# Performance work log

Measured on AMD Instinct MI355X. Metric: run time of the kernel, lower is better.

## Reference

```python
import jax, jax.numpy as jnp
import numpy as np

B, C, T = 8, 512, 8192
NQ, CBS, CBD = 9, 1024, 8
EPS = 1e-12  # F.normalize eps


def setup_inputs() -> dict:
    key = jax.random.key(0)
    ks = jax.random.split(key, 12)
    n = lambda i, shape, s: jax.random.normal(ks[i], shape, jnp.float32) * s
    return {
        "z": n(0, (B, C, T), 1.0),
        "down_w": n(1, (2, C, C, 2), 0.02),   # [layer, out, in, k] (torch Conv1d layout)
        "down_b": n(2, (2, C), 0.01),
        "up_w": n(3, (2, C, C, 2), 0.02),     # [layer, in, out, k] (torch ConvTranspose1d layout)
        "up_b": n(4, (2, C), 0.01),
        "in_v": n(5, (NQ, CBD, C), 0.05),     # weight_norm direction of in_proj 1x1 conv
        "in_g": 1.0 + n(6, (NQ, CBD), 0.02),  # weight_norm magnitude
        "in_b": n(7, (NQ, CBD), 0.01),
        "out_v": n(8, (NQ, C, CBD), 0.05),
        "out_g": 1.0 + n(9, (NQ, C), 0.02),
        "out_b": n(10, (NQ, C), 0.01),
        "codebooks": n(11, (NQ, CBS, CBD), 1.0),
    }


def _wn(g, v):
    # weight_norm (dim=0): per-output-row rescale
    return g[:, None] * v / jnp.linalg.norm(v, axis=1, keepdims=True)


def _l2norm(x):
    return x / jnp.maximum(jnp.linalg.norm(x, axis=-1, keepdims=True), EPS)


def _forward(z, down_w, down_b, up_w, up_b, in_v, in_g, in_b, out_v, out_g, out_b, codebooks):
    # --- downsample: two Conv1d(k=2, s=2) ---
    x = z
    for l in range(2):
        b, c, t = x.shape
        xr = x.reshape(b, c, t // 2, 2)
        x = jnp.einsum('bitk,oik->bot', xr, down_w[l]) + down_b[l][None, :, None]

    residual = x
    z_q = jnp.zeros_like(x)
    commit_loss = jnp.float32(0.0)
    cb_loss = jnp.float32(0.0)
    codes = []
    for i in range(NQ):
        # in_proj 1x1 conv (weight-normed)
        w_in = _wn(in_g[i], in_v[i])                 # [CBD, C]
        z_e = jnp.einsum('bdt,cd->bct', residual, w_in) + in_b[i][None, :, None]  # [B, CBD, T']
        # decode_latents: L2-normalize + squared-euclid via matmul + argmax
        bt = z_e.shape[0] * z_e.shape[2]
        enc = z_e.transpose(0, 2, 1).reshape(bt, CBD)
        enc_n = _l2norm(enc)
        cbk = codebooks[i]
        cb_n = _l2norm(cbk)
        dist = ((enc_n ** 2).sum(1, keepdims=True)
                - 2.0 * enc_n @ cb_n.T
                + (cb_n ** 2).sum(1)[None, :])        # [B*T', CBS]
        idx = jnp.argmax(-dist, axis=1).reshape(z_e.shape[0], -1)  # [B, T']
        z_q_i = cbk[idx].transpose(0, 2, 1)           # [B, CBD, T'] (un-normalized codebook rows)
        # losses (eval: mask all-true -> per-batch mean over (1,2) then batch mean == global mean)
        commit_loss = commit_loss + ((z_e - jax.lax.stop_gradient(z_q_i)) ** 2).mean()
        cb_loss = cb_loss + ((z_q_i - jax.lax.stop_gradient(z_e)) ** 2).mean()
        # straight-through + out_proj 1x1 conv (weight-normed)
        z_st = z_e + jax.lax.stop_gradient(z_q_i - z_e)
        w_out = _wn(out_g[i], out_v[i])               # [C, CBD]
        z_q_out = jnp.einsum('bct,dc->bdt', z_st, w_out) + out_b[i][None, :, None]
        z_q = z_q + z_q_out
        residual = residual - z_q_out
        codes.append(idx)
    codes = jnp.stack(codes, axis=1)                  # [B, NQ, T']

    x = z_q
    for l in range(2):
        b, c, t = x.shape
        x = jnp.einsum('bit,iok->botk', x, up_w[l]).reshape(b, C, t * 2) + up_b[l][None, :, None]
    return x, codes, commit_loss, cb_loss


def reference(z, down_w, down_b, up_w, up_b, in_v, in_g, in_b, out_v, out_g, out_b, codebooks):
    return _forward(z, down_w, down_b, up_w, up_b, in_v, in_g, in_b, out_v, out_g, out_b, codebooks)
```

## Files before the change

kernel.cpp:

```cpp
#include <hip/hip_runtime.h>
#include <math.h>


using u16 = unsigned short;
typedef __attribute__((ext_vector_type(8))) short bf16x8;
typedef __attribute__((ext_vector_type(8))) u16 su16x8;
typedef __attribute__((ext_vector_type(4))) float f32x4;

constexpr int NQ = 9, CBS = 1024, CBD = 8;
constexpr int TQ = 2048;
constexpr int NTOK = 16384;
constexpr int APS = 1048576;
#define EPSN 1e-12f

constexpr size_t OFF_X2    = 0;
constexpr size_t OFF_E0T   = 8388608;
constexpr size_t OFF_Q     = 9568256;
constexpr size_t OFF_WD    = 10878976;
constexpr size_t OFF_WDP   = 11927552;
constexpr size_t OFF_WEFF  = 13500416;
constexpr size_t OFF_WX    = 14548992;
constexpr size_t OFF_WINN  = 14712832;
constexpr size_t OFF_WOUTS = 14749696;
constexpr size_t OFF_CBS   = 14790656;
constexpr size_t OFF_PT    = 14809088;
constexpr size_t OFF_BEFF  = 14811428;
constexpr size_t OFF_BSUM  = 14811500;
constexpr size_t OFF_BD    = 14812012;
constexpr size_t OFF_BUP   = 14812524;
constexpr size_t OFF_LOSS  = 14813548;

__global__ void prep_small1(const float* __restrict__ in_v, const float* __restrict__ in_g,
                            const float* __restrict__ out_v, const float* __restrict__ out_g,
                            const float* __restrict__ out_b, const float* __restrict__ codebooks,
                            const float* __restrict__ down_w, const float* __restrict__ down_b,
                            const float* __restrict__ up_w, const float* __restrict__ up_b,
                            float* __restrict__ ws) {
  int bid = blockIdx.x, tid = threadIdx.x;
  int wid4 = tid >> 6, lane = tid & 63;
  if (bid < 18) {
    int wid = bid * 4 + wid4;
    if (wid < 72) {
      const float* v = in_v + (size_t)wid * 512;
      float ss = 0.f;
      for (int c = lane; c < 512; c += 64) ss += v[c] * v[c];
      #pragma unroll
      for (int o = 32; o; o >>= 1) ss += __shfl_xor(ss, o);
      float sc = in_g[wid] / sqrtf(ss);
      float* dst = ws + OFF_WINN + (size_t)wid * 512;
      for (int c = lane; c < 512; c += 64) dst[c] = v[c] * sc;
    }
  } else if (bid < 36) {
    int r = (bid - 18) * 256 + tid;
    if (r < 4608) {
      int i = r >> 9, c = r & 511;
      const float* v = out_v + (size_t)r * 8;
      float ss = 0.f;
      #pragma unroll
      for (int d = 0; d < 8; d++) ss += v[d] * v[d];
      float sc = out_g[r] / sqrtf(ss);
      float* dst = ws + OFF_WOUTS + (size_t)c * 80 + i * 8;
      #pragma unroll
      for (int d = 0; d < 8; d++) dst[d] = v[d] * sc;
    }
  } else if (bid < 72) {
    int r = (bid - 36) * 256 + tid;
    if (r < 9216) {
      int i = r >> 10, j = r & 1023;
      const float* v = codebooks + (size_t)r * 8;
      float ss = 0.f;
      #pragma unroll
      for (int d = 0; d < 8; d++) ss += v[d] * v[d];
      float nm = fmaxf(sqrtf(ss), EPSN);
      float nsq = 0.f;
      #pragma unroll
      for (int d = 0; d < 8; d++) { float cn = v[d] / nm; nsq += cn * cn; }
      ws[OFF_CBS + ((size_t)i * 2 + 0) * 1024 + j] = 2.0f / nm;
      ws[OFF_CBS + ((size_t)i * 2 + 1) * 1024 + j] = nsq;
    }
  } else if (bid < 74) {
    int c = (bid - 72) * 256 + tid;
    if (c < 512) {
      float s = 0.f;
      #pragma unroll
      for (int j = 0; j < 9; j++) s += out_b[j * 512 + c];
      ws[OFF_BSUM + c] = s;
      ws[OFF_WOUTS + (size_t)c * 80 + 72] = s;
      #pragma unroll
      for (int d = 73; d < 80; d++) ws[OFF_WOUTS + (size_t)c * 80 + d] = 0.f;
    }
  } else if (bid < 202) {
    int o = (bid - 74) * 4 + wid4;
    float s = 0.f;
    for (int m = lane; m < 512; m += 64) {
      float w0 = down_w[524288 + (size_t)o * 1024 + m * 2];
      float w1 = down_w[524288 + (size_t)o * 1024 + m * 2 + 1];
      s += (w0 + w1) * down_b[m];
    }
    #pragma unroll
    for (int off = 32; off; off >>= 1) s += __shfl_xor(s, off);
    if (lane == 0) ws[OFF_BD + o] = s + down_b[512 + o];
  } else {
    int gw = (bid - 202) * 256 + tid;
    int c = gw >> 1, j2 = gw & 1;
    float s = 0.f;
    for (int m = 0; m < 512; m++)
      s += up_w[524288 + (size_t)m * 1024 + c * 2 + j2] * up_b[m];
    ws[OFF_BUP + gw] = s + up_b[512 + c];
  }
}

__global__ void prep2(const float* __restrict__ in_b, const float* __restrict__ out_b,
                      float* __restrict__ ws) {
  int gw = blockIdx.x * 4 + (threadIdx.x >> 6), lane = threadIdx.x & 63;
  const float* WinN = ws + OFF_WINN;
  const float* WoutS = ws + OFF_WOUTS;
  if (gw < 2304) {
    int tri = gw >> 6, dd = gw & 63;
    int ip = 1;
    while (tri >= ip * (ip + 1) / 2) ip++;
    int i = tri - ip * (ip - 1) / 2;
    int d = dd >> 3, dp = dd & 7;
    const float* a = WinN + (size_t)(ip * 8 + d) * 512;
    float s = 0.f;
    for (int c = lane; c < 512; c += 64) s += a[c] * WoutS[(size_t)c * 80 + i * 8 + dp];
    #pragma unroll
    for (int o = 32; o; o >>= 1) s += __shfl_xor(s, o);
    if (lane == 0) ws[OFF_PT + (size_t)tri * 65 + dd] = s;
  } else if (gw < 2376) {
    int r = gw - 2304;
    int i = r >> 3;
    const float* a = WinN + (size_t)r * 512;
    float s = 0.f;
    for (int c = lane; c < 512; c += 64) {
      float ob = 0.f;
      for (int j = 0; j < i; j++) ob += out_b[j * 512 + c];
      s += a[c] * ob;
    }
    #pragma unroll
    for (int o = 32; o; o >>= 1) s += __shfl_xor(s, o);
    if (lane == 0) ws[OFF_BEFF + r] = in_b[r] - s;
  }
}

__global__ __launch_bounds__(256) void smallmm2(const float* __restrict__ down_w,
                                                const float* __restrict__ up_w,
                                                float* __restrict__ wd,
                                                float* __restrict__ weff) {
  __shared__ float As[32][68];
  __shared__ float Bs[32][68];
  const int tid = threadIdx.x;
  const int tx = tid & 15, ty = tid >> 4;
  const int b0 = blockIdx.x * 64, a0 = blockIdx.y * 64;
  const int which = blockIdx.z >> 2, j = blockIdx.z & 3;
  const int jh = j >> 1, jl = j & 1;
  const float* src = which ? up_w : down_w;
  float acc[4][4];
  #pragma unroll
  for (int i = 0; i < 4; i++)
    #pragma unroll
    for (int k = 0; k < 4; k++) acc[i][k] = 0.f;

  for (int k0 = 0; k0 < 512; k0 += 32) {
    #pragma unroll
    for (int rep = 0; rep < 8; rep++) {
      int f = tid + rep * 256;
      int aa = f >> 5, mm = f & 31;
      size_t ai = which ? (524288 + (size_t)(k0 + mm) * 1024 + (a0 + aa) * 2 + jl)
                        : (524288 + (size_t)(a0 + aa) * 1024 + (k0 + mm) * 2 + jh);
      As[mm][aa] = src[ai];
      int mm2 = f >> 6, bb = f & 63;
      size_t bi = which ? ((size_t)(b0 + bb) * 1024 + (k0 + mm2) * 2 + jh)
                        : ((size_t)(k0 + mm2) * 1024 + (b0 + bb) * 2 + jl);
      Bs[mm2][bb] = src[bi];
    }
    __syncthreads();
    #pragma unroll
    for (int kk = 0; kk < 32; kk++) {
      float av[4], bv[4];
      #pragma unroll
      for (int i = 0; i < 4; i++) av[i] = As[kk][ty * 4 + i];
      #pragma unroll
      for (int i = 0; i < 4; i++) bv[i] = Bs[kk][tx * 4 + i];
      #pragma unroll
      for (int i = 0; i < 4; i++)
        #pragma unroll
        for (int k = 0; k < 4; k++) acc[i][k] = fmaf(av[i], bv[k], acc[i][k]);
    }
    __syncthreads();
  }
  #pragma unroll
  for (int i = 0; i < 4; i++) {
    int a = a0 + ty * 4 + i;
    #pragma unroll
    for (int k = 0; k < 4; k++) {
      int b = b0 + tx * 4 + k;
      if (which) weff[((size_t)a * 4 + j) * 512 + b] = acc[i][k];
      else       wd[(size_t)a * 2048 + b * 4 + j] = acc[i][k];
    }
  }
}

__global__ __launch_bounds__(256) void prep_split_wx(const float* __restrict__ wd,
                                                     u16* __restrict__ wdp,
                                                     const float* __restrict__ weff,
                                                     const float* __restrict__ wouts,
                                                     float* __restrict__ wx) {
  const int tid = threadIdx.x;
  if (blockIdx.x < 4096) {
    int idx = blockIdx.x * 256 + tid;
    float v = wd[idx];
    unsigned u = __float_as_uint(v);
    wdp[idx] = (u16)(u >> 16);
    float r = v - __uint_as_float(u & 0xFFFF0000u);
    unsigned ur = __float_as_uint(r);
    wdp[APS + idx] = (u16)(ur >> 16);
    float r2 = r - __uint_as_float(ur & 0xFFFF0000u);
    wdp[2 * APS + idx] = (u16)(__float_as_uint(r2) >> 16);
    return;
  }
  __shared__ float Wes[16][512];
  __shared__ float WSs[64][80];
  const int m0 = (blockIdx.x - 4096) * 16;
  #pragma unroll
  for (int rep = 0; rep < 32; rep++) {
    int f = tid + rep * 256;
    Wes[f >> 9][f & 511] = weff[(size_t)(m0 + (f >> 9)) * 512 + (f & 511)];
  }
  const int rowq = tid >> 4, rq = tid & 15;
  float accs[5] = {0.f, 0.f, 0.f, 0.f, 0.f};
  for (int k0 = 0; k0 < 512; k0 += 64) {
    __syncthreads();
    #pragma unroll
    for (int rep = 0; rep < 20; rep++) {
      int f = tid + rep * 256;
      int kk = f / 80, col = f % 80;
      WSs[kk][col] = wouts[(size_t)(k0 + kk) * 80 + col];
    }
    __syncthreads();
    #pragma unroll 4
    for (int kk = 0; kk < 64; kk++) {
      float we = Wes[rowq][k0 + kk];
      #pragma unroll
      for (int s = 0; s < 5; s++) accs[s] = fmaf(we, WSs[kk][rq + 16 * s], accs[s]);
    }
  }
  #pragma unroll
  for (int s = 0; s < 5; s++) {
    int r = rq + 16 * s;
    if (r < 73) wx[(size_t)(m0 + rowq) * 80 + r] = accs[s];
  }
  if (tid < 112) {
    int row = tid / 7, col = 73 + tid % 7;
    wx[(size_t)(m0 + row) * 80 + col] = 0.f;
  }
}

__global__ __launch_bounds__(256) void gemm_down(const u16* __restrict__ Ap,
                                                 const float* __restrict__ z,
                                                 const float* __restrict__ bias,
                                                 float* __restrict__ Out) {
  constexpr int NS = 3, K = 2048;
  __shared__ u16 Bp[2][NS][128][32];
  const int tid = threadIdx.x;
  const int w = tid >> 6, l = tid & 63;
  const int g = l >> 4, li = l & 15;
  const int wr = w >> 1, wc = w & 1;
  const int n0 = blockIdx.x * 128, m0 = blockIdx.y * 128;
  const int nn = tid & 127, kw = tid >> 7;
  const int bb = n0 >> 11;
  const int tb = (n0 & 2047) + nn;

  f32x4 acc[4][4];
  #pragma unroll
  for (int a = 0; a < 4; a++)
    #pragma unroll
    for (int b = 0; b < 4; b++) acc[a][b] = (f32x4){0.f, 0.f, 0.f, 0.f};

  float pvA[16], pvB[16];

#define LOADB(PV, K0)                                                           \
  {                                                                             \
    int c0_ = ((K0) >> 2) + kw * 4;                                             \
    _Pragma("unroll")                                                           \
    for (int cc_ = 0; cc_ < 4; ++cc_)                                           \
      *(float4*)&PV[4 * cc_] =                                                  \
          *(const float4*)(z + ((size_t)(bb * 512 + c0_ + cc_) << 13) + 4 * tb);\
  }

  const int sw = (nn >> 1) & 3;
  const int c0 = ((2 * kw) ^ sw) << 3, c1 = ((2 * kw + 1) ^ sw) << 3;

#define STAGE(BUF, PV)                                                          \
  {                                                                             \
    su16x8 pa_[NS], pb_[NS];                                                    \
    _Pragma("unroll")                                                           \
    for (int j_ = 0; j_ < 8; ++j_) {                                            \
      {                                                                         \
        float v_ = PV[j_];                                                      \
        unsigned u_ = __float_as_uint(v_);                                      \
        pa_[0][j_] = (u16)(u_ >> 16);                                           \
        float r_ = v_ - __uint_as_float(u_ & 0xFFFF0000u);                      \
        unsigned ur_ = __float_as_uint(r_);                                     \
        pa_[1][j_] = (u16)(ur_ >> 16);                                          \
        float r2_ = r_ - __uint_as_float(ur_ & 0xFFFF0000u);                    \
        pa_[2][j_] = (u16)(__float_as_uint(r2_) >> 16);                         \
      }                                                                         \
      {                                                                         \
        float v_ = PV[8 + j_];                                                  \
        unsigned u_ = __float_as_uint(v_);                                      \
        pb_[0][j_] = (u16)(u_ >> 16);                                           \
        float r_ = v_ - __uint_as_float(u_ & 0xFFFF0000u);                      \
        unsigned ur_ = __float_as_uint(r_);                                     \
        pb_[1][j_] = (u16)(ur_ >> 16);                                          \
        float r2_ = r_ - __uint_as_float(ur_ & 0xFFFF0000u);                    \
        pb_[2][j_] = (u16)(__float_as_uint(r2_) >> 16);                         \
      }                                                                         \
    }                                                                           \
    _Pragma("unroll")                                                           \
    for (int p_ = 0; p_ < NS; ++p_) {                                           \
      *(su16x8*)&Bp[BUF][p_][nn][c0] = pa_[p_];                                 \
      *(su16x8*)&Bp[BUF][p_][nn][c1] = pb_[p_];                                 \
    }                                                                           \
  }

#define COMPUTE(BUF, K0)                                                        \
  {                                                                             \
    bf16x8 bfr_[4][NS];                                                         \
    _Pragma("unroll")                                                           \
    for (int fn_ = 0; fn_ < 4; ++fn_) {                                         \
      int row_ = wc * 64 + fn_ * 16 + li;                                       \
      int cs_ = ((g ^ ((row_ >> 1) & 3)) << 3);                                 \
      _Pragma("unroll")                                                         \
      for (int q_ = 0; q_ < NS; ++q_)                                           \
        bfr_[fn_][q_] = *(const bf16x8*)&Bp[BUF][q_][row_][cs_];                \
    }                                                                           \
    const u16* arow_ = Ap + (size_t)(m0 + wr * 64 + li) * K + (K0) + g * 8;     \
    _Pragma("unroll")                                                           \
    for (int fm_ = 0; fm_ < 4; ++fm_) {                                         \
      bf16x8 afr_[NS];                                                          \
      _Pragma("unroll")                                                         \
      for (int p_ = 0; p_ < NS; ++p_)                                           \
        afr_[p_] = *(const bf16x8*)(arow_ + (size_t)p_ * APS + (size_t)fm_ * 16 * K); \
      _Pragma("unroll")                                                         \
      for (int fn_ = 0; fn_ < 4; ++fn_) {                                       \
        f32x4 a_ = acc[fm_][fn_];                                               \
        a_ = __builtin_amdgcn_mfma_f32_16x16x32_bf16(afr_[2], bfr_[fn_][0], a_, 0, 0, 0); \
        a_ = __builtin_amdgcn_mfma_f32_16x16x32_bf16(afr_[1], bfr_[fn_][1], a_, 0, 0, 0); \
        a_ = __builtin_amdgcn_mfma_f32_16x16x32_bf16(afr_[0], bfr_[fn_][2], a_, 0, 0, 0); \
        a_ = __builtin_amdgcn_mfma_f32_16x16x32_bf16(afr_[1], bfr_[fn_][0], a_, 0, 0, 0); \
        a_ = __builtin_amdgcn_mfma_f32_16x16x32_bf16(afr_[0], bfr_[fn_][1], a_, 0, 0, 0); \
        a_ = __builtin_amdgcn_mfma_f32_16x16x32_bf16(afr_[0], bfr_[fn_][0], a_, 0, 0, 0); \
        acc[fm_][fn_] = a_;                                                     \
      }                                                                         \
    }                                                                           \
  }

  LOADB(pvA, 0)
  LOADB(pvB, 32)
  STAGE(0, pvA)
  LOADB(pvA, 64)
  __syncthreads();

  for (int k0 = 0; k0 < K; k0 += 64) {
    STAGE(1, pvB)
    if (k0 + 96 < K) { LOADB(pvB, k0 + 96) }
    COMPUTE(0, k0)
    __syncthreads();
    if (k0 + 64 < K) { STAGE(0, pvA) }
    if (k0 + 128 < K) { LOADB(pvA, k0 + 128) }
    COMPUTE(1, k0 + 32)
    __syncthreads();
  }
#undef LOADB
#undef STAGE
#undef COMPUTE

  const int mb = m0 + wr * 64 + g * 4;
  const int nb = n0 + wc * 64 + li;
  #pragma unroll
  for (int fn = 0; fn < 4; ++fn) {
    int n = nb + fn * 16;
    int b = n >> 11, t = n & 2047;
    #pragma unroll
    for (int fm = 0; fm < 4; ++fm)
      #pragma unroll
      for (int r = 0; r < 4; ++r) {
        int o = mb + fm * 16 + r;
        Out[((size_t)((b << 9) + o)) * 2048 + t] = acc[fm][fn][r] + bias[o];
      }
  }
}

__global__ __launch_bounds__(256) void gemm_e0f(const float* __restrict__ A,
                                                const float* __restrict__ Bsrc,
                                                float* __restrict__ e0t) {
  constexpr int M = 72, K = 512, Tt = 2048;
  __shared__ float As[16][132];
  __shared__ float Bs[16][68];
  int tid = threadIdx.x;
  int tx = tid & 7, ty = tid >> 3;
  int n0 = blockIdx.x * 64;
  int b = n0 / Tt, t0 = n0 % Tt;
  float acc[4][8];
  #pragma unroll
  for (int i = 0; i < 4; i++)
    #pragma unroll
    for (int j = 0; j < 8; j++) acc[i][j] = 0.f;

  for (int k0 = 0; k0 < K; k0 += 16) {
    #pragma unroll
    for (int rep = 0; rep < 2; rep++) {
      int f = tid + rep * 256;
      int row = f >> 2, c4 = (f & 3) << 2;
      int m = row, k = k0 + c4;
      float4 v = make_float4(0.f, 0.f, 0.f, 0.f);
      if (m < M) v = *(const float4*)(A + (size_t)m * K + k);
      As[c4 + 0][row] = v.x; As[c4 + 1][row] = v.y;
      As[c4 + 2][row] = v.z; As[c4 + 3][row] = v.w;
    }
    {
      int kk = tid >> 4, n4 = (tid & 15) << 2;
      float4 v = *(const float4*)(Bsrc + ((size_t)(b * K + k0 + kk)) * Tt + t0 + n4);
      *(float4*)&Bs[kk][n4] = v;
    }
    __syncthreads();
    #pragma unroll
    for (int kk = 0; kk < 16; kk++) {
      float a[4], bb[8];
      #pragma unroll
      for (int i = 0; i < 4; i++) a[i] = As[kk][ty * 4 + i];
      *(float4*)&bb[0] = *(float4*)&Bs[kk][tx * 8];
      *(float4*)&bb[4] = *(float4*)&Bs[kk][tx * 8 + 4];
      #pragma unroll
      for (int i = 0; i < 4; i++)
        #pragma unroll
        for (int j = 0; j < 8; j++) acc[i][j] = fmaf(a[i], bb[j], acc[i][j]);
    }
    __syncthreads();
  }
  #pragma unroll
  for (int j = 0; j < 8; j++) {
    int n = n0 + tx * 8 + j;
    #pragma unroll
    for (int i = 0; i < 4; i++) {
      int m = ty * 4 + i;
      if (m < M) e0t[(size_t)n * M + m] = acc[i][j];
    }
  }
}

__global__ __launch_bounds__(256) void xfin(const float* __restrict__ wx,
                                            const float* __restrict__ Q,
                                            const float* __restrict__ bup,
                                            float* __restrict__ xout) {
  __shared__ float Wxs[128][80];
  __shared__ float Qs[128][80];
  const int tid = threadIdx.x;
  const int n0 = blockIdx.x * 128, m0 = blockIdx.y * 128;
  #pragma unroll
  for (int rep = 0; rep < 10; rep++) {
    int f = tid + rep * 256;
    *(float4*)&Wxs[0][f * 4] = *(const float4*)(wx + (size_t)m0 * 80 + f * 4);
    *(float4*)&Qs[0][f * 4] = *(const float4*)(Q + (size_t)n0 * 80 + f * 4);
  }
  __syncthreads();

  const int txn = tid & 15, tym = tid >> 4;
  float acc[8][8];
  #pragma unroll
  for (int i = 0; i < 8; i++)
    #pragma unroll
    for (int j = 0; j < 8; j++) acc[i][j] = 0.f;

  #pragma unroll 2
  for (int r4 = 0; r4 < 18; r4++) {
    float4 wv[8], qv[8];
    #pragma unroll
    for (int i = 0; i < 8; i++) wv[i] = *(const float4*)&Wxs[tym * 8 + i][r4 * 4];
    #pragma unroll
    for (int j = 0; j < 8; j++) qv[j] = *(const float4*)&Qs[txn * 8 + j][r4 * 4];
    #pragma unroll
    for (int i = 0; i < 8; i++)
      #pragma unroll
      for (int j = 0; j < 8; j++) {
        acc[i][j] = fmaf(wv[i].x, qv[j].x, acc[i][j]);
        acc[i][j] = fmaf(wv[i].y, qv[j].y, acc[i][j]);
        acc[i][j] = fmaf(wv[i].z, qv[j].z, acc[i][j]);
        acc[i][j] = fmaf(wv[i].w, qv[j].w, acc[i][j]);
      }
  }

  float bxv[8];
  #pragma unroll
  for (int mi = 0; mi < 8; mi++) {
    int mp = m0 + tym * 8 + mi;
    bxv[mi] = Wxs[tym * 8 + mi][72] + bup[(mp >> 2) * 2 + (mp & 1)];
  }
  #pragma unroll
  for (int cg = 0; cg < 2; cg++) {
    int mp0 = m0 + tym * 8 + cg * 4;
    int c = mp0 >> 2;
    #pragma unroll
    for (int j = 0; j < 8; j++) {
      int n = n0 + txn * 8 + j;
      int b = n >> 11, t = n & 2047;
      float4 sv = make_float4(acc[cg * 4 + 0][j] + bxv[cg * 4 + 0],
                              acc[cg * 4 + 1][j] + bxv[cg * 4 + 1],
                              acc[cg * 4 + 2][j] + bxv[cg * 4 + 2],
                              acc[cg * 4 + 3][j] + bxv[cg * 4 + 3]);
      *(float4*)&xout[((size_t)((b << 9) + c)) * 8192 + 4 * t] = sv;
    }
  }
}

__global__ __launch_bounds__(256) void rvq_kernel(const float* __restrict__ codebooks,
                                                  const float* __restrict__ e0t,
                                                  const float* __restrict__ cbsW,
                                                  const float* __restrict__ ptW,
                                                  const float* __restrict__ beffW,
                                                  float* __restrict__ Qout,
                                                  float* __restrict__ codesOut,
                                                  float* __restrict__ lossPart) {
  __shared__ float cbv[8][1024];
  __shared__ float cbs2[2][1024];
  __shared__ float est[16][72];
  __shared__ float lred[4];
  int tid = threadIdx.x, wid = tid >> 6, lane = tid & 63;
  int nb0 = blockIdx.x * 16;
  for (int idx = tid; idx < 16 * 72; idx += 256)
    est[idx / 72][idx % 72] = e0t[(size_t)nb0 * 72 + idx] + beffW[idx % 72];
  float lossLocal = 0.f;

  for (int i = 0; i < NQ; i++) {
    __syncthreads();
    const float* cbg = codebooks + (size_t)i * CBS * CBD;
    for (int lin = tid; lin < 2048; lin += 256) {
      int j = lin >> 1, half = (lin & 1) << 2;
      float4 v = *(const float4*)(cbg + (size_t)j * 8 + half);
      cbv[half + 0][j] = v.x; cbv[half + 1][j] = v.y;
      cbv[half + 2][j] = v.z; cbv[half + 3][j] = v.w;
    }
    for (int lin = tid; lin < 1024; lin += 256) {
      cbs2[0][lin] = cbsW[((size_t)i * 2 + 0) * 1024 + lin];
      cbs2[1][lin] = cbsW[((size_t)i * 2 + 1) * 1024 + lin];
    }
    __syncthreads();

    float ze[4][8], en[4][8];
    #pragma unroll
    for (int w = 0; w < 4; w++) {
      int tokl = wid * 4 + w;
      float ss = 0.f;
      #pragma unroll
      for (int d = 0; d < 8; d++) { float v = est[tokl][i * 8 + d]; ze[w][d] = v; ss += v * v; }
      float inv = 1.0f / fmaxf(sqrtf(ss), EPSN);
      #pragma unroll
      for (int d = 0; d < 8; d++) en[w][d] = ze[w][d] * inv;
    }
    float best[4]; int bidx[4];
    #pragma unroll
    for (int w = 0; w < 4; w++) { best[w] = -INFINITY; bidx[w] = 0; }
    #pragma unroll 4
    for (int r = 0; r < 16; r++) {
      int j = lane + (r << 6);
      float c0 = cbv[0][j], c1 = cbv[1][j], c2 = cbv[2][j], c3 = cbv[3][j];
      float c4 = cbv[4][j], c5 = cbv[5][j], c6 = cbv[6][j], c7 = cbv[7][j];
      float ti = cbs2[0][j], ns = cbs2[1][j];
      #pragma unroll
      for (int w = 0; w < 4; w++) {
        float dt = en[w][0] * c0;
        dt = fmaf(en[w][1], c1, dt); dt = fmaf(en[w][2], c2, dt);
        dt = fmaf(en[w][3], c3, dt); dt = fmaf(en[w][4], c4, dt);
        dt = fmaf(en[w][5], c5, dt); dt = fmaf(en[w][6], c6, dt);
        dt = fmaf(en[w][7], c7, dt);
        float s = fmaf(dt, ti, -ns);
        if (s > best[w]) { best[w] = s; bidx[w] = j; }
      }
    }
    #pragma unroll
    for (int w = 0; w < 4; w++) {
      #pragma unroll
      for (int off = 32; off; off >>= 1) {
        float so = __shfl_xor(best[w], off);
        int jo = __shfl_xor(bidx[w], off);
        if (so > best[w] || (so == best[w] && jo < bidx[w])) { best[w] = so; bidx[w] = jo; }
      }
    }
    int d = lane & 7;
    #pragma unroll
    for (int w = 0; w < 4; w++) {
      int jstar = bidx[w];
      int tokl = wid * 4 + w;
      int n = nb0 + tokl;
      float qd = cbv[d][jstar];
      float diff = ze[w][d] - qd;
      float sq = diff * diff;
      sq += __shfl_xor(sq, 1); sq += __shfl_xor(sq, 2); sq += __shfl_xor(sq, 4);
      if (lane == 0) lossLocal += sq;
      if (lane < 8) Qout[(size_t)n * 80 + i * 8 + lane] = qd;
      if (lane == 0) codesOut[(size_t)((n >> 11) * NQ + i) * TQ + (n & (TQ - 1))] = (float)jstar;
      if (i < NQ - 1) {
        int f = lane >> 3, d2 = lane & 7;
        int ip = i + 1 + f;
        if (ip < NQ) {
          int tri = (ip * (ip - 1)) / 2 + i;
          const float* prow = ptW + (size_t)tri * 65 + d2 * 8;
          float s = 0.f;
          #pragma unroll
          for (int dp = 0; dp < 8; dp++) s = fmaf(prow[dp], cbv[dp][jstar], s);
          est[tokl][ip * 8 + d2] -= s;
        }
      }
    }
  }
  if (lane == 0) lred[wid] = lossLocal;
  __syncthreads();
  if (tid == 0) {
    float s = ((lred[0] + lred[1]) + lred[2]) + lred[3];
    lossPart[blockIdx.x] = s;
  }
}

__global__ void loss_fin(const float* __restrict__ lossPart, float* __restrict__ out) {
  __shared__ float s[256];
  int tid = threadIdx.x;
  float v = 0.f;
  for (int r = 0; r < 4; r++) v += lossPart[tid + r * 256];
  s[tid] = v;
  __syncthreads();
  for (int w = 128; w; w >>= 1) {
    if (tid < w) s[tid] += s[tid + w];
    __syncthreads();
  }
  if (tid == 0) {
    float total = s[0] / 131072.0f;
    out[0] = total;
    out[1] = total;
  }
}

extern "C" void kernel_launch(void* const* d_in, const int* in_sizes, int n_in,
                              void* d_out, int out_size, void* d_ws, size_t ws_size,
                              hipStream_t stream) {
  const float* z      = (const float*)d_in[0];
  const float* down_w = (const float*)d_in[1];
  const float* down_b = (const float*)d_in[2];
  const float* up_w   = (const float*)d_in[3];
  const float* up_b   = (const float*)d_in[4];
  const float* in_v   = (const float*)d_in[5];
  const float* in_g   = (const float*)d_in[6];
  const float* in_b   = (const float*)d_in[7];
  const float* out_v  = (const float*)d_in[8];
  const float* out_g  = (const float*)d_in[9];
  const float* out_b  = (const float*)d_in[10];
  const float* codebooks = (const float*)d_in[11];
  float* ws = (float*)d_ws;
  float* xout = (float*)d_out;
  float* codesOut = xout + (size_t)8 * 512 * 8192;
  float* lossOut = codesOut + (size_t)8 * NQ * TQ;

  hipLaunchKernelGGL(prep_small1, dim3(206), dim3(256), 0, stream,
                     in_v, in_g, out_v, out_g, out_b, codebooks,
                     down_w, down_b, up_w, up_b, ws);
  hipLaunchKernelGGL(prep2, dim3(594), dim3(256), 0, stream, in_b, out_b, ws);
  hipLaunchKernelGGL(smallmm2, dim3(8, 8, 8), dim3(256), 0, stream,
                     down_w, up_w, ws + OFF_WD, ws + OFF_WEFF);
  hipLaunchKernelGGL(prep_split_wx, dim3(4224), dim3(256), 0, stream,
                     ws + OFF_WD, (u16*)(ws + OFF_WDP),
                     ws + OFF_WEFF, ws + OFF_WOUTS, ws + OFF_WX);
  hipLaunchKernelGGL(gemm_down, dim3(128, 4), dim3(256), 0, stream,
                     (const u16*)(ws + OFF_WDP), z, ws + OFF_BD, ws + OFF_X2);
  hipLaunchKernelGGL(gemm_e0f, dim3(256), dim3(256), 0, stream,
                     ws + OFF_WINN, ws + OFF_X2, ws + OFF_E0T);
  hipLaunchKernelGGL(rvq_kernel, dim3(1024), dim3(256), 0, stream,
                     codebooks, ws + OFF_E0T, ws + OFF_CBS, ws + OFF_PT, ws + OFF_BEFF,
                     ws + OFF_Q, codesOut, ws + OFF_LOSS);
  hipLaunchKernelGGL(xfin, dim3(128, 16), dim3(256), 0, stream,
                     ws + OFF_WX, ws + OFF_Q, ws + OFF_BUP, xout);
  hipLaunchKernelGGL(loss_fin, dim3(1), dim3(256), 0, stream, ws + OFF_LOSS, lossOut);
}
```

Before: 780.4 us.

## Merge prep kernels, fold in_proj GEMM into RVQ, fuse loss into xfin

```diff
diff --git a/kernel.cpp b/kernel.cpp
--- a/kernel.cpp
+++ b/kernel.cpp
@@ -14,7 +14,6 @@
 #define EPSN 1e-12f
 
 constexpr size_t OFF_X2    = 0;
-constexpr size_t OFF_E0T   = 8388608;
 constexpr size_t OFF_Q     = 9568256;
 constexpr size_t OFF_WD    = 10878976;
 constexpr size_t OFF_WDP   = 11927552;
@@ -30,129 +29,99 @@
 constexpr size_t OFF_BUP   = 14812524;
 constexpr size_t OFF_LOSS  = 14813548;
 
-__global__ void prep_small1(const float* __restrict__ in_v, const float* __restrict__ in_g,
-                            const float* __restrict__ out_v, const float* __restrict__ out_g,
-                            const float* __restrict__ out_b, const float* __restrict__ codebooks,
-                            const float* __restrict__ down_w, const float* __restrict__ down_b,
-                            const float* __restrict__ up_w, const float* __restrict__ up_b,
-                            float* __restrict__ ws) {
+__global__ __launch_bounds__(256) void prep_all1(const float* __restrict__ in_v,
+                                                 const float* __restrict__ in_g,
+                                                 const float* __restrict__ out_v,
+                                                 const float* __restrict__ out_g,
+                                                 const float* __restrict__ out_b,
+                                                 const float* __restrict__ codebooks,
+                                                 const float* __restrict__ down_w,
+                                                 const float* __restrict__ down_b,
+                                                 const float* __restrict__ up_w,
+                                                 const float* __restrict__ up_b,
+                                                 float* __restrict__ ws) {
   int bid = blockIdx.x, tid = threadIdx.x;
-  int wid4 = tid >> 6, lane = tid & 63;
-  if (bid < 18) {
-    int wid = bid * 4 + wid4;
-    if (wid < 72) {
-      const float* v = in_v + (size_t)wid * 512;
-      float ss = 0.f;
-      for (int c = lane; c < 512; c += 64) ss += v[c] * v[c];
-      #pragma unroll
-      for (int o = 32; o; o >>= 1) ss += __shfl_xor(ss, o);
-      float sc = in_g[wid] / sqrtf(ss);
-      float* dst = ws + OFF_WINN + (size_t)wid * 512;
-      for (int c = lane; c < 512; c += 64) dst[c] = v[c] * sc;
-    }
-  } else if (bid < 36) {
-    int r = (bid - 18) * 256 + tid;
-    if (r < 4608) {
-      int i = r >> 9, c = r & 511;
-      const float* v = out_v + (size_t)r * 8;
-      float ss = 0.f;
-      #pragma unroll
-      for (int d = 0; d < 8; d++) ss += v[d] * v[d];
-      float sc = out_g[r] / sqrtf(ss);
-      float* dst = ws + OFF_WOUTS + (size_t)c * 80 + i * 8;
-      #pragma unroll
-      for (int d = 0; d < 8; d++) dst[d] = v[d] * sc;
-    }
-  } else if (bid < 72) {
-    int r = (bid - 36) * 256 + tid;
-    if (r < 9216) {
-      int i = r >> 10, j = r & 1023;
-      const float* v = codebooks + (size_t)r * 8;
-      float ss = 0.f;
-      #pragma unroll
-      for (int d = 0; d < 8; d++) ss += v[d] * v[d];
-      float nm = fmaxf(sqrtf(ss), EPSN);
-      float nsq = 0.f;
-      #pragma unroll
-      for (int d = 0; d < 8; d++) { float cn = v[d] / nm; nsq += cn * cn; }
-      ws[OFF_CBS + ((size_t)i * 2 + 0) * 1024 + j] = 2.0f / nm;
-      ws[OFF_CBS + ((size_t)i * 2 + 1) * 1024 + j] = nsq;
-    }
-  } else if (bid < 74) {
-    int c = (bid - 72) * 256 + tid;
-    if (c < 512) {
+  if (bid < 206) {
+    int wid4 = tid >> 6, lane = tid & 63;
+    if (bid < 18) {
+      int wid = bid * 4 + wid4;
+      if (wid < 72) {
+        const float* v = in_v + (size_t)wid * 512;
+        float ss = 0.f;
+        for (int c = lane; c < 512; c += 64) ss += v[c] * v[c];
+        #pragma unroll
+        for (int o = 32; o; o >>= 1) ss += __shfl_xor(ss, o);
+        float sc = in_g[wid] / sqrtf(ss);
+        float* dst = ws + OFF_WINN + (size_t)wid * 512;
+        for (int c = lane; c < 512; c += 64) dst[c] = v[c] * sc;
+      }
+    } else if (bid < 36) {
+      int r = (bid - 18) * 256 + tid;
+      if (r < 4608) {
+        int i = r >> 9, c = r & 511;
+        const float* v = out_v + (size_t)r * 8;
+        float ss = 0.f;
+        #pragma unroll
+        for (int d = 0; d < 8; d++) ss += v[d] * v[d];
+        float sc = out_g[r] / sqrtf(ss);
+        float* dst = ws + OFF_WOUTS + (size_t)c * 80 + i * 8;
+        #pragma unroll
+        for (int d = 0; d < 8; d++) dst[d] = v[d] * sc;
+      }
+    } else if (bid < 72) {
+      int r = (bid - 36) * 256 + tid;
+      if (r < 9216) {
+        int i = r >> 10, j = r & 1023;
+        const float* v = codebooks + (size_t)r * 8;
+        float ss = 0.f;
+        #pragma unroll
+        for (int d = 0; d < 8; d++) ss += v[d] * v[d];
+        float nm = fmaxf(sqrtf(ss), EPSN);
+        float nsq = 0.f;
+        #pragma unroll
+        for (int d = 0; d < 8; d++) { float cn = v[d] / nm; nsq += cn * cn; }
+        ws[OFF_CBS + ((size_t)i * 2 + 0) * 1024 + j] = 2.0f / nm;
+        ws[OFF_CBS + ((size_t)i * 2 + 1) * 1024 + j] = nsq;
+      }
+    } else if (bid < 74) {
+      int c = (bid - 72) * 256 + tid;
+      if (c < 512) {
+        float s = 0.f;
+        #pragma unroll
+        for (int j = 0; j < 9; j++) s += out_b[j * 512 + c];
+        ws[OFF_BSUM + c] = s;
+        ws[OFF_WOUTS + (size_t)c * 80 + 72] = s;
+        #pragma unroll
+        for (int d = 73; d < 80; d++) ws[OFF_WOUTS + (size_t)c * 80 + d] = 0.f;
+      }
+    } else if (bid < 202) {
+      int o = (bid - 74) * 4 + wid4;
       float s = 0.f;
-      #pragma unroll
-      for (int j = 0; j < 9; j++) s += out_b[j * 512 + c];
-      ws[OFF_BSUM + c] = s;
-      ws[OFF_WOUTS + (size_t)c * 80 + 72] = s;
-      #pragma unroll
-      for (int d = 73; d < 80; d++) ws[OFF_WOUTS + (size_t)c * 80 + d] = 0.f;
-    }
-  } else if (bid < 202) {
-    int o = (bid - 74) * 4 + wid4;
-    float s = 0.f;
-    for (int m = lane; m < 512; m += 64) {
-      float w0 = down_w[524288 + (size_t)o * 1024 + m * 2];
-      float w1 = down_w[524288 + (size_t)o * 1024 + m * 2 + 1];
-      s += (w0 + w1) * down_b[m];
-    }
-    #pragma unroll
-    for (int off = 32; off; off >>= 1) s += __shfl_xor(s, off);
-    if (lane == 0) ws[OFF_BD + o] = s + down_b[512 + o];
-  } else {
-    int gw = (bid - 202) * 256 + tid;
-    int c = gw >> 1, j2 = gw & 1;
-    float s = 0.f;
-    for (int m = 0; m < 512; m++)
-      s += up_w[524288 + (size_t)m * 1024 + c * 2 + j2] * up_b[m];
-    ws[OFF_BUP + gw] = s + up_b[512 + c];
-  }
-}
-
-__global__ void prep2(const float* __restrict__ in_b, const float* __restrict__ out_b,
-                      float* __restrict__ ws) {
-  int gw = blockIdx.x * 4 + (threadIdx.x >> 6), lane = threadIdx.x & 63;
-  const float* WinN = ws + OFF_WINN;
-  const float* WoutS = ws + OFF_WOUTS;
-  if (gw < 2304) {
-    int tri = gw >> 6, dd = gw & 63;
-    int ip = 1;
-    while (tri >= ip * (ip + 1) / 2) ip++;
-    int i = tri - ip * (ip - 1) / 2;
-    int d = dd >> 3, dp = dd & 7;
-    const float* a = WinN + (size_t)(ip * 8 + d) * 512;
-    float s = 0.f;
-    for (int c = lane; c < 512; c += 64) s += a[c] * WoutS[(size_t)c * 80 + i * 8 + dp];
-    #pragma unroll
-    for (int o = 32; o; o >>= 1) s += __shfl_xor(s, o);
-    if (lane == 0) ws[OFF_PT + (size_t)tri * 65 + dd] = s;
-  } else if (gw < 2376) {
-    int r = gw - 2304;
-    int i = r >> 3;
-    const float* a = WinN + (size_t)r * 512;
-    float s = 0.f;
-    for (int c = lane; c < 512; c += 64) {
-      float ob = 0.f;
-      for (int j = 0; j < i; j++) ob += out_b[j * 512 + c];
-      s += a[c] * ob;
-    }
-    #pragma unroll
-    for (int o = 32; o; o >>= 1) s += __shfl_xor(s, o);
-    if (lane == 0) ws[OFF_BEFF + r] = in_b[r] - s;
-  }
-}
-
-__global__ __launch_bounds__(256) void smallmm2(const float* __restrict__ down_w,
-                                                const float* __restrict__ up_w,
-                                                float* __restrict__ wd,
-                                                float* __restrict__ weff) {
+      for (int m = lane; m < 512; m += 64) {
+        float w0 = down_w[524288 + (size_t)o * 1024 + m * 2];
+        float w1 = down_w[524288 + (size_t)o * 1024 + m * 2 + 1];
+        s += (w0 + w1) * down_b[m];
+      }
+      #pragma unroll
+      for (int off = 32; off; off >>= 1) s += __shfl_xor(s, off);
+      if (lane == 0) ws[OFF_BD + o] = s + down_b[512 + o];
+    } else {
+      int gw = (bid - 202) * 256 + tid;
+      int c = gw >> 1, j2 = gw & 1;
+      float s = 0.f;
+      for (int m = 0; m < 512; m++)
+        s += up_w[524288 + (size_t)m * 1024 + c * 2 + j2] * up_b[m];
+      ws[OFF_BUP + gw] = s + up_b[512 + c];
+    }
+    return;
+  }
   __shared__ float As[32][68];
   __shared__ float Bs[32][68];
-  const int tid = threadIdx.x;
+  const int bid2 = bid - 206;
   const int tx = tid & 15, ty = tid >> 4;
-  const int b0 = blockIdx.x * 64, a0 = blockIdx.y * 64;
-  const int which = blockIdx.z >> 2, j = blockIdx.z & 3;
+  const int b0 = (bid2 & 7) * 64, a0 = ((bid2 >> 3) & 7) * 64;
+  const int zz = bid2 >> 6;
+  const int which = zz >> 2, j = zz & 3;
   const int jh = j >> 1, jl = j & 1;
   const float* src = which ? up_w : down_w;
   float acc[4][4];
@@ -189,6 +158,8 @@
     }
     __syncthreads();
   }
+  float* wd = ws + OFF_WD;
+  float* weff = ws + OFF_WEFF;
   #pragma unroll
   for (int i = 0; i < 4; i++) {
     int a = a0 + ty * 4 + i;
@@ -201,14 +172,47 @@
   }
 }
 
-__global__ __launch_bounds__(256) void prep_split_wx(const float* __restrict__ wd,
-                                                     u16* __restrict__ wdp,
-                                                     const float* __restrict__ weff,
-                                                     const float* __restrict__ wouts,
-                                                     float* __restrict__ wx) {
+__global__ __launch_bounds__(256) void prep_all2(const float* __restrict__ in_b,
+                                                 const float* __restrict__ out_b,
+                                                 float* __restrict__ ws) {
   const int tid = threadIdx.x;
-  if (blockIdx.x < 4096) {
-    int idx = blockIdx.x * 256 + tid;
+  if (blockIdx.x < 594) {
+    int gw = blockIdx.x * 4 + (tid >> 6), lane = tid & 63;
+    const float* WinN = ws + OFF_WINN;
+    const float* WoutS = ws + OFF_WOUTS;
+    if (gw < 2304) {
+      int tri = gw >> 6, dd = gw & 63;
+      int ip = 1;
+      while (tri >= ip * (ip + 1) / 2) ip++;
+      int i = tri - ip * (ip - 1) / 2;
+      int d = dd >> 3, dp = dd & 7;
+      const float* a = WinN + (size_t)(ip * 8 + d) * 512;
+      float s = 0.f;
+      for (int c = lane; c < 512; c += 64) s += a[c] * WoutS[(size_t)c * 80 + i * 8 + dp];
+      #pragma unroll
+      for (int o = 32; o; o >>= 1) s += __shfl_xor(s, o);
+      if (lane == 0) ws[OFF_PT + (size_t)tri * 65 + dd] = s;
+    } else if (gw < 2376) {
+      int r = gw - 2304;
+      int i = r >> 3;
+      const float* a = WinN + (size_t)r * 512;
+      float s = 0.f;
+      for (int c = lane; c < 512; c += 64) {
+        float ob = 0.f;
+        for (int j = 0; j < i; j++) ob += out_b[j * 512 + c];
+        s += a[c] * ob;
+      }
+      #pragma unroll
+      for (int o = 32; o; o >>= 1) s += __shfl_xor(s, o);
+      if (lane == 0) ws[OFF_BEFF + r] = in_b[r] - s;
+    }
+    return;
+  }
+  const int bid2 = blockIdx.x - 594;
+  if (bid2 < 4096) {
+    int idx = bid2 * 256 + tid;
+    const float* wd = ws + OFF_WD;
+    u16* wdp = (u16*)(ws + OFF_WDP);
     float v = wd[idx];
     unsigned u = __float_as_uint(v);
     wdp[idx] = (u16)(u >> 16);
@@ -221,7 +225,10 @@
   }
   __shared__ float Wes[16][512];
   __shared__ float WSs[64][80];
-  const int m0 = (blockIdx.x - 4096) * 16;
+  const float* weff = ws + OFF_WEFF;
+  const float* wouts = ws + OFF_WOUTS;
+  float* wx = ws + OFF_WX;
+  const int m0 = (bid2 - 4096) * 16;
   #pragma unroll
   for (int rep = 0; rep < 32; rep++) {
     int f = tid + rep * 256;
@@ -392,130 +399,9 @@
   }
 }
 
-__global__ __launch_bounds__(256) void gemm_e0f(const float* __restrict__ A,
-                                                const float* __restrict__ Bsrc,
-                                                float* __restrict__ e0t) {
-  constexpr int M = 72, K = 512, Tt = 2048;
-  __shared__ float As[16][132];
-  __shared__ float Bs[16][68];
-  int tid = threadIdx.x;
-  int tx = tid & 7, ty = tid >> 3;
-  int n0 = blockIdx.x * 64;
-  int b = n0 / Tt, t0 = n0 % Tt;
-  float acc[4][8];
-  #pragma unroll
-  for (int i = 0; i < 4; i++)
-    #pragma unroll
-    for (int j = 0; j < 8; j++) acc[i][j] = 0.f;
-
-  for (int k0 = 0; k0 < K; k0 += 16) {
-    #pragma unroll
-    for (int rep = 0; rep < 2; rep++) {
-      int f = tid + rep * 256;
-      int row = f >> 2, c4 = (f & 3) << 2;
-      int m = row, k = k0 + c4;
-      float4 v = make_float4(0.f, 0.f, 0.f, 0.f);
-      if (m < M) v = *(const float4*)(A + (size_t)m * K + k);
-      As[c4 + 0][row] = v.x; As[c4 + 1][row] = v.y;
-      As[c4 + 2][row] = v.z; As[c4 + 3][row] = v.w;
-    }
-    {
-      int kk = tid >> 4, n4 = (tid & 15) << 2;
-      float4 v = *(const float4*)(Bsrc + ((size_t)(b * K + k0 + kk)) * Tt + t0 + n4);
-      *(float4*)&Bs[kk][n4] = v;
-    }
-    __syncthreads();
-    #pragma unroll
-    for (int kk = 0; kk < 16; kk++) {
-      float a[4], bb[8];
-      #pragma unroll
-      for (int i = 0; i < 4; i++) a[i] = As[kk][ty * 4 + i];
-      *(float4*)&bb[0] = *(float4*)&Bs[kk][tx * 8];
-      *(float4*)&bb[4] = *(float4*)&Bs[kk][tx * 8 + 4];
-      #pragma unroll
-      for (int i = 0; i < 4; i++)
-        #pragma unroll
-        for (int j = 0; j < 8; j++) acc[i][j] = fmaf(a[i], bb[j], acc[i][j]);
-    }
-    __syncthreads();
-  }
-  #pragma unroll
-  for (int j = 0; j < 8; j++) {
-    int n = n0 + tx * 8 + j;
-    #pragma unroll
-    for (int i = 0; i < 4; i++) {
-      int m = ty * 4 + i;
-      if (m < M) e0t[(size_t)n * M + m] = acc[i][j];
-    }
-  }
-}
-
-__global__ __launch_bounds__(256) void xfin(const float* __restrict__ wx,
-                                            const float* __restrict__ Q,
-                                            const float* __restrict__ bup,
-                                            float* __restrict__ xout) {
-  __shared__ float Wxs[128][80];
-  __shared__ float Qs[128][80];
-  const int tid = threadIdx.x;
-  const int n0 = blockIdx.x * 128, m0 = blockIdx.y * 128;
-  #pragma unroll
-  for (int rep = 0; rep < 10; rep++) {
-    int f = tid + rep * 256;
-    *(float4*)&Wxs[0][f * 4] = *(const float4*)(wx + (size_t)m0 * 80 + f * 4);
-    *(float4*)&Qs[0][f * 4] = *(const float4*)(Q + (size_t)n0 * 80 + f * 4);
-  }
-  __syncthreads();
-
-  const int txn = tid & 15, tym = tid >> 4;
-  float acc[8][8];
-  #pragma unroll
-  for (int i = 0; i < 8; i++)
-    #pragma unroll
-    for (int j = 0; j < 8; j++) acc[i][j] = 0.f;
-
-  #pragma unroll 2
-  for (int r4 = 0; r4 < 18; r4++) {
-    float4 wv[8], qv[8];
-    #pragma unroll
-    for (int i = 0; i < 8; i++) wv[i] = *(const float4*)&Wxs[tym * 8 + i][r4 * 4];
-    #pragma unroll
-    for (int j = 0; j < 8; j++) qv[j] = *(const float4*)&Qs[txn * 8 + j][r4 * 4];
-    #pragma unroll
-    for (int i = 0; i < 8; i++)
-      #pragma unroll
-      for (int j = 0; j < 8; j++) {
-        acc[i][j] = fmaf(wv[i].x, qv[j].x, acc[i][j]);
-        acc[i][j] = fmaf(wv[i].y, qv[j].y, acc[i][j]);
-        acc[i][j] = fmaf(wv[i].z, qv[j].z, acc[i][j]);
-        acc[i][j] = fmaf(wv[i].w, qv[j].w, acc[i][j]);
-      }
-  }
-
-  float bxv[8];
-  #pragma unroll
-  for (int mi = 0; mi < 8; mi++) {
-    int mp = m0 + tym * 8 + mi;
-    bxv[mi] = Wxs[tym * 8 + mi][72] + bup[(mp >> 2) * 2 + (mp & 1)];
-  }
-  #pragma unroll
-  for (int cg = 0; cg < 2; cg++) {
-    int mp0 = m0 + tym * 8 + cg * 4;
-    int c = mp0 >> 2;
-    #pragma unroll
-    for (int j = 0; j < 8; j++) {
-      int n = n0 + txn * 8 + j;
-      int b = n >> 11, t = n & 2047;
-      float4 sv = make_float4(acc[cg * 4 + 0][j] + bxv[cg * 4 + 0],
-                              acc[cg * 4 + 1][j] + bxv[cg * 4 + 1],
-                              acc[cg * 4 + 2][j] + bxv[cg * 4 + 2],
-                              acc[cg * 4 + 3][j] + bxv[cg * 4 + 3]);
-      *(float4*)&xout[((size_t)((b << 9) + c)) * 8192 + 4 * t] = sv;
-    }
-  }
-}
-
 __global__ __launch_bounds__(256) void rvq_kernel(const float* __restrict__ codebooks,
-                                                  const float* __restrict__ e0t,
+                                                  const float* __restrict__ x2,
+                                                  const float* __restrict__ winn,
                                                   const float* __restrict__ cbsW,
                                                   const float* __restrict__ ptW,
                                                   const float* __restrict__ beffW,
@@ -528,8 +414,18 @@
   __shared__ float lred[4];
   int tid = threadIdx.x, wid = tid >> 6, lane = tid & 63;
   int nb0 = blockIdx.x * 16;
-  for (int idx = tid; idx < 16 * 72; idx += 256)
-    est[idx / 72][idx % 72] = e0t[(size_t)nb0 * 72 + idx] + beffW[idx % 72];
+
+  for (int idx = tid; idx < 1152; idx += 256) {
+    int m = idx >> 4, tokl = idx & 15;
+    int n = nb0 + tokl;
+    int b = n >> 11, t = n & 2047;
+    const float* xcol = x2 + ((size_t)b * 512) * 2048 + t;
+    const float* wrow = winn + (size_t)m * 512;
+    float acc = 0.f;
+    for (int k = 0; k < 512; ++k)
+      acc = fmaf(wrow[k], xcol[(size_t)k * 2048], acc);
+    est[tokl][m] = acc + beffW[m];
+  }
   float lossLocal = 0.f;
 
   for (int i = 0; i < NQ; i++) {
@@ -622,21 +518,87 @@
   }
 }
 
-__global__ void loss_fin(const float* __restrict__ lossPart, float* __restrict__ out) {
-  __shared__ float s[256];
-  int tid = threadIdx.x;
-  float v = 0.f;
-  for (int r = 0; r < 4; r++) v += lossPart[tid + r * 256];
-  s[tid] = v;
+__global__ __launch_bounds__(256) void xfin_loss(const float* __restrict__ wx,
+                                                 const float* __restrict__ Q,
+                                                 const float* __restrict__ bup,
+                                                 const float* __restrict__ lossPart,
+                                                 float* __restrict__ xout,
+                                                 float* __restrict__ lossOut) {
+  const int tid = threadIdx.x;
+  if (blockIdx.x == 128) {
+    if (blockIdx.y != 0) return;
+    __shared__ float s[256];
+    float v = 0.f;
+    for (int r = 0; r < 4; r++) v += lossPart[tid + r * 256];
+    s[tid] = v;
+    __syncthreads();
+    for (int w = 128; w; w >>= 1) {
+      if (tid < w) s[tid] += s[tid + w];
+      __syncthreads();
+    }
+    if (tid == 0) {
+      float total = s[0] / 131072.0f;
+      lossOut[0] = total;
+      lossOut[1] = total;
+    }
+    return;
+  }
+  __shared__ float Wxs[128][80];
+  __shared__ float Qs[128][80];
+  const int n0 = blockIdx.x * 128, m0 = blockIdx.y * 128;
+  #pragma unroll
+  for (int rep = 0; rep < 10; rep++) {
+    int f = tid + rep * 256;
+    *(float4*)&Wxs[0][f * 4] = *(const float4*)(wx + (size_t)m0 * 80 + f * 4);
+    *(float4*)&Qs[0][f * 4] = *(const float4*)(Q + (size_t)n0 * 80 + f * 4);
+  }
   __syncthreads();
-  for (int w = 128; w; w >>= 1) {
-    if (tid < w) s[tid] += s[tid + w];
-    __syncthreads();
-  }
-  if (tid == 0) {
-    float total = s[0] / 131072.0f;
-    out[0] = total;
-    out[1] = total;
+
+  const int txn = tid & 15, tym = tid >> 4;
+  float acc[8][8];
+  #pragma unroll
+  for (int i = 0; i < 8; i++)
+    #pragma unroll
+    for (int j = 0; j < 8; j++) acc[i][j] = 0.f;
+
+  #pragma unroll 2
+  for (int r4 = 0; r4 < 18; r4++) {
+    float4 wv[8], qv[8];
+    #pragma unroll
+    for (int i = 0; i < 8; i++) wv[i] = *(const float4*)&Wxs[tym * 8 + i][r4 * 4];
+    #pragma unroll
+    for (int j = 0; j < 8; j++) qv[j] = *(const float4*)&Qs[txn * 8 + j][r4 * 4];
+    #pragma unroll
+    for (int i = 0; i < 8; i++)
+      #pragma unroll
+      for (int j = 0; j < 8; j++) {
+        acc[i][j] = fmaf(wv[i].x, qv[j].x, acc[i][j]);
+        acc[i][j] = fmaf(wv[i].y, qv[j].y, acc[i][j]);
+        acc[i][j] = fmaf(wv[i].z, qv[j].z, acc[i][j]);
+        acc[i][j] = fmaf(wv[i].w, qv[j].w, acc[i][j]);
+      }
+  }
+
+  float bxv[8];
+  #pragma unroll
+  for (int mi = 0; mi < 8; mi++) {
+    int mp = m0 + tym * 8 + mi;
+    bxv[mi] = Wxs[tym * 8 + mi][72] + bup[(mp >> 2) * 2 + (mp & 1)];
+  }
+  #pragma unroll
+  for (int cg = 0; cg < 2; cg++) {
+    int mp0 = m0 + tym * 8 + cg * 4;
+    int c = mp0 >> 2;
+    #pragma unroll
+    for (int j = 0; j < 8; j++) {
+      int n = n0 + txn * 8 + j;
+      int b = n >> 11, t = n & 2047;
+      float4 sv = make_float4(acc[cg * 4 + 0][j] + bxv[cg * 4 + 0],
+                              acc[cg * 4 + 1][j] + bxv[cg * 4 + 1],
+                              acc[cg * 4 + 2][j] + bxv[cg * 4 + 2],
+                              acc[cg * 4 + 3][j] + bxv[cg * 4 + 3]);
+      *(float4*)&xout[((size_t)((b << 9) + c)) * 8192 + 4 * t] = sv;
+    }
   }
 }
 
@@ -660,23 +622,17 @@
   float* codesOut = xout + (size_t)8 * 512 * 8192;
   float* lossOut = codesOut + (size_t)8 * NQ * TQ;
 
-  hipLaunchKernelGGL(prep_small1, dim3(206), dim3(256), 0, stream,
+  hipLaunchKernelGGL(prep_all1, dim3(718), dim3(256), 0, stream,
                      in_v, in_g, out_v, out_g, out_b, codebooks,
                      down_w, down_b, up_w, up_b, ws);
-  hipLaunchKernelGGL(prep2, dim3(594), dim3(256), 0, stream, in_b, out_b, ws);
-  hipLaunchKernelGGL(smallmm2, dim3(8, 8, 8), dim3(256), 0, stream,
-                     down_w, up_w, ws + OFF_WD, ws + OFF_WEFF);
-  hipLaunchKernelGGL(prep_split_wx, dim3(4224), dim3(256), 0, stream,
-                     ws + OFF_WD, (u16*)(ws + OFF_WDP),
-                     ws + OFF_WEFF, ws + OFF_WOUTS, ws + OFF_WX);
+  hipLaunchKernelGGL(prep_all2, dim3(4818), dim3(256), 0, stream, in_b, out_b, ws);
   hipLaunchKernelGGL(gemm_down, dim3(128, 4), dim3(256), 0, stream,
                      (const u16*)(ws + OFF_WDP), z, ws + OFF_BD, ws + OFF_X2);
-  hipLaunchKernelGGL(gemm_e0f, dim3(256), dim3(256), 0, stream,
-                     ws + OFF_WINN, ws + OFF_X2, ws + OFF_E0T);
   hipLaunchKernelGGL(rvq_kernel, dim3(1024), dim3(256), 0, stream,
-                     codebooks, ws + OFF_E0T, ws + OFF_CBS, ws + OFF_PT, ws + OFF_BEFF,
+                     codebooks, ws + OFF_X2, ws + OFF_WINN,
+                     ws + OFF_CBS, ws + OFF_PT, ws + OFF_BEFF,
                      ws + OFF_Q, codesOut, ws + OFF_LOSS);
-  hipLaunchKernelGGL(xfin, dim3(128, 16), dim3(256), 0, stream,
-                     ws + OFF_WX, ws + OFF_Q, ws + OFF_BUP, xout);
-  hipLaunchKernelGGL(loss_fin, dim3(1), dim3(256), 0, stream, ws + OFF_LOSS, lossOut);
+  hipLaunchKernelGGL(xfin_loss, dim3(129, 16), dim3(256), 0, stream,
+                     ws + OFF_WX, ws + OFF_Q, ws + OFF_BUP, ws + OFF_LOSS,
+                     xout, lossOut);
 }
```

Measured after the change: 915.0 us. 17.2% more time.
